# Optimization experiments

Hardware: AMD Instinct MI355X
Metric: run time of the kernel (lower is better)

The kernel has to match this reference:

```python
import jax, jax.numpy as jnp
import numpy as np


def _lap_mul(A, x):
    # L @ x with L = D^{-1/2} A D^{-1/2}, D = diag(rowsum(A))
    d = 1.0 / jnp.sqrt(jnp.sum(A, axis=-1))  # [N]
    return d[:, None] * (A @ (d[:, None] * x))


def setup_inputs() -> dict:
    key = jax.random.key(0)
    k1, k2, k3, k4, k5, k6 = jax.random.split(key, 6)
    N, D_IN, D_OUT = 4096, 128, 128
    x = jax.random.normal(k1, (N, D_IN), dtype=jnp.float32)
    A = jax.random.uniform(k2, (N, N), dtype=jnp.float32)
    # linear params stored as [in, out] (apply via x @ W + b)
    s1 = 1.0 / np.sqrt(D_IN)
    W1 = jax.random.uniform(k3, (D_IN, D_OUT), minval=-s1, maxval=s1, dtype=jnp.float32)
    b1 = jax.random.uniform(k4, (D_OUT,), minval=-s1, maxval=s1, dtype=jnp.float32)
    W2 = jax.random.uniform(k5, (D_IN, D_OUT), minval=-s1, maxval=s1, dtype=jnp.float32)
    b2 = jax.random.uniform(k6, (D_OUT,), minval=-s1, maxval=s1, dtype=jnp.float32)
    return {"x": x, "A": A, "W1": W1, "b1": b1, "W2": W2, "b2": b2, "sigma": 1, "k": 4}


def reference(x, A, W1, b1, W2, b2, sigma, k):
    # first graph conv + linear1 + leaky relu
    z = _lap_mul(A, x) @ W1 + b1            # [N, d_out]
    z = jax.nn.leaky_relu(z, negative_slope=0.1)

    # pairwise Euclidean distance (efficient cdist form, same math as the
    # original broadcasted (z_i - z_j)**2 sum, without the d x N x N blowup)
    sq = jnp.sum(z * z, axis=-1)            # [N]
    d2 = sq[:, None] + sq[None, :] - 2.0 * (z @ z.T)
    d2 = jnp.maximum(d2, 0.0)
    S = jnp.sqrt(d2 + 1e-10)                # [N, N]
    S = jnp.exp(-S / (2.0 * sigma))

    # double-argsort rank -> keep top-k per row (emulates original masking)
    order = jnp.argsort(-S, axis=-1)
    ranks = jnp.argsort(order, axis=-1)
    S = jnp.where(ranks < k, S, 0.0)

    A2 = S + A
    out = _lap_mul(A2, x) @ W2 + b2         # [N, d_out]
    return out
```

## Files before the change

### kernel.cpp

```cpp
#include <hip/hip_runtime.h>
#include <cstdint>
#include <cstddef>

#define NN 4096
#define DD 128

using short8 = __attribute__((ext_vector_type(8))) short;
using f32x4  = __attribute__((ext_vector_type(4))) float;
typedef unsigned long long u64;

typedef __attribute__((address_space(1))) void gvoid;
typedef __attribute__((address_space(3))) void lvoid;

__device__ __forceinline__ void async16(const void* g, void* l) {
  __builtin_amdgcn_global_load_lds((gvoid*)g, (lvoid*)l, 16, 0, 0);
}

__device__ __forceinline__ float dec_f(const void* p) {
  if (!p) return 1.0f;
  int b = *(const int*)p;
  return (b >= 0 && b < 1000000) ? (float)b : __int_as_float(b);
}
__device__ __forceinline__ int dec_i(const void* p) {
  if (!p) return 4;
  int b = *(const int*)p;
  return (b >= 0 && b < 1000000) ? b : (int)__int_as_float(b);
}

__device__ __forceinline__ unsigned short f2bf(float f) {
  union { float f; unsigned int u; } v; v.f = f;
  unsigned int u = v.u;
  unsigned int r = (u + 0x7fffu + ((u >> 16) & 1u)) >> 16;
  return (unsigned short)r;
}
__device__ __forceinline__ float bf2f(unsigned short h) {
  union { unsigned int u; float f; } v; v.u = ((unsigned int)h) << 16;
  return v.f;
}

__device__ __forceinline__ void ins4(u64 (&l)[4], u64 k) {
#pragma unroll
  for (int t = 0; t < 4; ++t) {
    u64 old = l[t];
    bool bt = k < old;
    l[t] = bt ? k : old;
    k = bt ? old : k;
  }
}

template <int ROWS, int KC, int NTHR>
__device__ __forceinline__ void stage2(const unsigned short* src, int row0, int kb,
                                       unsigned short* dst, int tid, int stride) {
  const int CPR = KC / 8;
  const int ITER = (ROWS * CPR) / NTHR;
#pragma unroll
  for (int t = 0; t < ITER; ++t) {
    int id = tid + t * NTHR;
    int r = id / CPR;
    int p = id % CPR;
    int lc = p ^ (r & 7);
    const void* g = src + (size_t)(row0 + r) * stride + kb + lc * 8;
    async16(g, dst + (size_t)(id & ~63) * 8);
  }
}

template <int CPR>
__device__ __forceinline__ short8 fragN(const unsigned short* t, int row, int ch) {
  return *(const short8*)(t + (size_t)(row * CPR + (ch ^ (row & 7))) * 8);
}

__global__ __launch_bounds__(256) void k_rowsum_scale(
    const float* __restrict__ A, const float* __restrict__ x,
    float* __restrict__ rowsumA, float* __restrict__ dvec, float* __restrict__ V,
    unsigned short* __restrict__ Ah, unsigned short* __restrict__ Al) {
  int row = blockIdx.x;
  int tid = threadIdx.x;
  const float4* Arow = (const float4*)(A + (size_t)row * NN);
  float s = 0.f;
#pragma unroll
  for (int l = 0; l < 4; ++l) {
    int idx = tid + l * 256;
    float4 v = Arow[idx];
    s += (v.x + v.y) + (v.z + v.w);
    if (Ah) {
      ushort4 h = {f2bf(v.x), f2bf(v.y), f2bf(v.z), f2bf(v.w)};
      *(ushort4*)(Ah + (size_t)row * NN + idx * 4) = h;
      if (Al) {
        ushort4 lo = {f2bf(v.x - bf2f(h.x)), f2bf(v.y - bf2f(h.y)),
                      f2bf(v.z - bf2f(h.z)), f2bf(v.w - bf2f(h.w))};
        *(ushort4*)(Al + (size_t)row * NN + idx * 4) = lo;
      }
    }
  }
  __shared__ float red[256];
  __shared__ float dsh;
  red[tid] = s;
  __syncthreads();
  if (tid < 64) {
    s = red[tid] + red[tid + 64] + red[tid + 128] + red[tid + 192];
#pragma unroll
    for (int off = 32; off > 0; off >>= 1) s += __shfl_down(s, off, 64);
    if (tid == 0) { rowsumA[row] = s; float d = rsqrtf(s); dvec[row] = d; dsh = d; }
  }
  __syncthreads();
  float d = dsh;
  if (tid < 32) {
    float4 xv = ((const float4*)(x + (size_t)row * DD))[tid];
    float4 o; o.x = d * xv.x; o.y = d * xv.y; o.z = d * xv.z; o.w = d * xv.w;
    ((float4*)(V + (size_t)row * DD))[tid] = o;
  }
}

__global__ __launch_bounds__(256) void k_vt(
    const float* __restrict__ V, unsigned short* __restrict__ VTh,
    unsigned short* __restrict__ VTl, int emit_lo) {
  __shared__ float Ls[64 * 132];
  int bx = blockIdx.x, tid = threadIdx.x;
  int r0 = bx * 64;
#pragma unroll
  for (int l = 0; l < 8; ++l) {
    int idx = tid + l * 256;
    int r = idx >> 5, c4 = (idx & 31) << 2;
    *(float4*)(Ls + r * 132 + c4) = *(const float4*)(V + (size_t)(r0 + r) * DD + c4);
  }
  __syncthreads();
  int c = tid >> 1, rh = tid & 1;
  unsigned short hb[32], lb[32];
#pragma unroll
  for (int i = 0; i < 32; ++i) {
    float v = Ls[(rh * 32 + i) * 132 + c];
    hb[i] = f2bf(v);
    lb[i] = f2bf(v - bf2f(hb[i]));
  }
  size_t base = (size_t)c * NN + r0 + rh * 32;
#pragma unroll
  for (int q = 0; q < 8; ++q) {
    ushort4 h = {hb[q * 4], hb[q * 4 + 1], hb[q * 4 + 2], hb[q * 4 + 3]};
    *(ushort4*)(VTh + base + q * 4) = h;
  }
  if (emit_lo) {
#pragma unroll
    for (int q = 0; q < 8; ++q) {
      ushort4 lo = {lb[q * 4], lb[q * 4 + 1], lb[q * 4 + 2], lb[q * 4 + 3]};
      *(ushort4*)(VTl + base + q * 4) = lo;
    }
  }
}

template <int TERMS>
__global__ __launch_bounds__(256) void k_gemm_bf16(
    const unsigned short* __restrict__ Ah, const unsigned short* __restrict__ Al,
    const unsigned short* __restrict__ Bh, const unsigned short* __restrict__ Bl,
    float* __restrict__ G) {
  __shared__ __align__(16) unsigned short As_h[128 * 64];
  __shared__ __align__(16) unsigned short Bs_h[128 * 64];
  __shared__ __align__(16) unsigned short As_l[TERMS == 3 ? 128 * 64 : 8];
  __shared__ __align__(16) unsigned short Bs_l[TERMS == 3 ? 128 * 64 : 8];

  int bx = blockIdx.x;
  int mt = bx >> 4, sp = bx & 15;
  int m0 = mt * 128;
  int ks = sp * 256;
  int tid = threadIdx.x, lane = tid & 63, w = tid >> 6;
  int wm = w >> 1, wn = w & 1;
  int l15 = lane & 15, quad = lane >> 4;

  f32x4 acc[4][4];
#pragma unroll
  for (int a = 0; a < 4; ++a)
#pragma unroll
    for (int b = 0; b < 4; ++b) acc[a][b] = (f32x4){0.f, 0.f, 0.f, 0.f};

  for (int kt = 0; kt < 256; kt += 64) {
    int kb = ks + kt;
    __syncthreads();
    stage2<128, 64, 256>(Ah, m0, kb, As_h, tid, NN);
    stage2<128, 64, 256>(Bh, 0, kb, Bs_h, tid, NN);
    if (TERMS == 3) {
      stage2<128, 64, 256>(Al, m0, kb, As_l, tid, NN);
      stage2<128, 64, 256>(Bl, 0, kb, Bs_l, tid, NN);
    }
    __syncthreads();
#pragma unroll
    for (int k0 = 0; k0 < 64; k0 += 32) {
      int ch = (k0 >> 3) + quad;
      short8 a_h[4], b_h[4], a_l[4], b_l[4];
#pragma unroll
      for (int f = 0; f < 4; ++f) {
        int ra = wm * 64 + f * 16 + l15;
        int cb = wn * 64 + f * 16 + l15;
        a_h[f] = fragN<8>(As_h, ra, ch);
        b_h[f] = fragN<8>(Bs_h, cb, ch);
        if (TERMS == 3) { a_l[f] = fragN<8>(As_l, ra, ch); b_l[f] = fragN<8>(Bs_l, cb, ch); }
      }
#pragma unroll
      for (int fm = 0; fm < 4; ++fm)
#pragma unroll
        for (int fn = 0; fn < 4; ++fn) {
          acc[fm][fn] = __builtin_amdgcn_mfma_f32_16x16x32_bf16(a_h[fm], b_h[fn], acc[fm][fn], 0, 0, 0);
          if (TERMS == 3) {
            acc[fm][fn] = __builtin_amdgcn_mfma_f32_16x16x32_bf16(a_h[fm], b_l[fn], acc[fm][fn], 0, 0, 0);
            acc[fm][fn] = __builtin_amdgcn_mfma_f32_16x16x32_bf16(a_l[fm], b_h[fn], acc[fm][fn], 0, 0, 0);
          }
        }
    }
  }
  float* Gp = G + (size_t)sp * NN * DD;
#pragma unroll
  for (int fm = 0; fm < 4; ++fm) {
    int rb = m0 + wm * 64 + fm * 16 + quad * 4;
#pragma unroll
    for (int fn = 0; fn < 4; ++fn) {
      int c = wn * 64 + fn * 16 + l15;
#pragma unroll
      for (int i = 0; i < 4; ++i)
        Gp[(size_t)(rb + i) * DD + c] = acc[fm][fn][i];
    }
  }
}

__global__ __launch_bounds__(256) void k_gemm_av(
    const float* __restrict__ A, const float* __restrict__ V,
    float* __restrict__ G, int ksplit) {
  int bx = blockIdx.x;
  int mt = bx & 63;
  int sp = bx >> 6;
  int m0 = mt * 64;
  int klen = NN / ksplit;
  int k0 = sp * klen;
  int tid = threadIdx.x;
  int tr = tid >> 4, tc = tid & 15;
  __shared__ float As[64 * 68];
  __shared__ float Bs[64 * 128];
  float acc[4][8];
#pragma unroll
  for (int r = 0; r < 4; ++r)
#pragma unroll
    for (int c = 0; c < 8; ++c) acc[r][c] = 0.f;
  for (int kt = 0; kt < klen; kt += 64) {
    int kb = k0 + kt;
    __syncthreads();
#pragma unroll
    for (int l = 0; l < 4; ++l) {
      int idx = tid + l * 256;
      int r = idx >> 4;
      int kq = (idx & 15) << 2;
      float4 a = *(const float4*)(A + (size_t)(m0 + r) * NN + kb + kq);
      As[(kq + 0) * 68 + r] = a.x;
      As[(kq + 1) * 68 + r] = a.y;
      As[(kq + 2) * 68 + r] = a.z;
      As[(kq + 3) * 68 + r] = a.w;
    }
#pragma unroll
    for (int l = 0; l < 8; ++l) {
      int idx = tid + l * 256;
      int kr = idx >> 5;
      int c4 = (idx & 31) << 2;
      *(float4*)(Bs + kr * 128 + c4) = *(const float4*)(V + (size_t)(kb + kr) * DD + c4);
    }
    __syncthreads();
#pragma unroll 8
    for (int kk = 0; kk < 64; ++kk) {
      float4 a = *(const float4*)(As + kk * 68 + tr * 4);
      float4 b0 = *(const float4*)(Bs + kk * 128 + tc * 8);
      float4 b1 = *(const float4*)(Bs + kk * 128 + tc * 8 + 4);
      float av[4] = {a.x, a.y, a.z, a.w};
      float bv[8] = {b0.x, b0.y, b0.z, b0.w, b1.x, b1.y, b1.z, b1.w};
#pragma unroll
      for (int r = 0; r < 4; ++r)
#pragma unroll
        for (int c = 0; c < 8; ++c) acc[r][c] = fmaf(av[r], bv[c], acc[r][c]);
    }
  }
  float* Gp = G + (size_t)sp * NN * DD;
#pragma unroll
  for (int r = 0; r < 4; ++r) {
    int gr = m0 + tr * 4 + r;
    float4 o0 = {acc[r][0], acc[r][1], acc[r][2], acc[r][3]};
    float4 o1 = {acc[r][4], acc[r][5], acc[r][6], acc[r][7]};
    *(float4*)(Gp + (size_t)gr * DD + tc * 8) = o0;
    *(float4*)(Gp + (size_t)gr * DD + tc * 8 + 4) = o1;
  }
}

template <int NP>
__global__ __launch_bounds__(256) void k_lin(
    const float* __restrict__ G,
    const float* __restrict__ W, const float* __restrict__ bvec,
    const float* __restrict__ dvec, float* __restrict__ Out,
    int leaky, float* __restrict__ sqout,
    unsigned short* __restrict__ zh, unsigned short* __restrict__ zl,
    const float* __restrict__ Vsp, const float* __restrict__ sval,
    const int* __restrict__ sidx, const void* kptr) {
  int bx = blockIdx.x;
  int r0 = bx * 16;
  int tid = threadIdx.x;
  int tr = tid >> 4, tc = tid & 15;
  __shared__ float Gs[16 * 132];
  __shared__ float Ws[32 * 128];
  __shared__ float red[256];
  __shared__ float ds[16];

#pragma unroll
  for (int l = 0; l < 8; ++l) {
    int idx = tid + l * 256;
    int r = idx >> 7;
    int c = idx & 127;
    float v = 0.f;
#pragma unroll
    for (int p = 0; p < NP; ++p)
      v += G[(size_t)p * NN * DD + (size_t)(r0 + r) * DD + c];
    Gs[r * 132 + c] = v;
  }
  if (tid < 16) ds[tid] = dvec[r0 + tid];

  if (sidx != nullptr) {
    __syncthreads();
    int kk = dec_i(kptr); kk = kk < 1 ? 1 : (kk > 4 ? 4 : kk);
    int gr = r0 + tr;
    float add[8] = {0, 0, 0, 0, 0, 0, 0, 0};
    for (int t = 0; t < kk; ++t) {
      float sv = sval[gr * 8 + t];
      int id = sidx[gr * 8 + t];
      const float4* vr = (const float4*)(Vsp + (size_t)id * DD);
      float4 w0 = vr[tc * 2], w1 = vr[tc * 2 + 1];
      add[0] = fmaf(sv, w0.x, add[0]); add[1] = fmaf(sv, w0.y, add[1]);
      add[2] = fmaf(sv, w0.z, add[2]); add[3] = fmaf(sv, w0.w, add[3]);
      add[4] = fmaf(sv, w1.x, add[4]); add[5] = fmaf(sv, w1.y, add[5]);
      add[6] = fmaf(sv, w1.z, add[6]); add[7] = fmaf(sv, w1.w, add[7]);
    }
#pragma unroll
    for (int u = 0; u < 8; ++u) Gs[tr * 132 + tc * 8 + u] += add[u];
  }

  float acc[8];
#pragma unroll
  for (int u = 0; u < 8; ++u) acc[u] = 0.f;

  for (int t0 = 0; t0 < 128; t0 += 32) {
    __syncthreads();
#pragma unroll
    for (int l = 0; l < 4; ++l) {
      int idx = tid + l * 256;
      int tt = idx >> 5;
      int c4 = (idx & 31) << 2;
      *(float4*)(Ws + tt * 128 + c4) = *(const float4*)(W + (size_t)(t0 + tt) * DD + c4);
    }
    __syncthreads();
#pragma unroll 8
    for (int tt = 0; tt < 32; ++tt) {
      float g = Gs[tr * 132 + t0 + tt];
      float4 w0 = *(const float4*)(Ws + tt * 128 + tc * 8);
      float4 w1 = *(const float4*)(Ws + tt * 128 + tc * 8 + 4);
      acc[0] = fmaf(g, w0.x, acc[0]); acc[1] = fmaf(g, w0.y, acc[1]);
      acc[2] = fmaf(g, w0.z, acc[2]); acc[3] = fmaf(g, w0.w, acc[3]);
      acc[4] = fmaf(g, w1.x, acc[4]); acc[5] = fmaf(g, w1.y, acc[5]);
      acc[6] = fmaf(g, w1.z, acc[6]); acc[7] = fmaf(g, w1.w, acc[7]);
    }
  }

  float d = ds[tr];
  float4 b0 = *(const float4*)(bvec + tc * 8);
  float4 b1 = *(const float4*)(bvec + tc * 8 + 4);
  float bb[8] = {b0.x, b0.y, b0.z, b0.w, b1.x, b1.y, b1.z, b1.w};
  float o[8];
#pragma unroll
  for (int u = 0; u < 8; ++u) {
    float v = fmaf(d, acc[u], bb[u]);
    if (leaky) v = v > 0.f ? v : 0.1f * v;
    o[u] = v;
  }
  size_t rowoff = (size_t)(r0 + tr) * DD + tc * 8;
  if (Out) {
    float4 o0 = {o[0], o[1], o[2], o[3]};
    float4 o1 = {o[4], o[5], o[6], o[7]};
    *(float4*)(Out + rowoff) = o0;
    *(float4*)(Out + rowoff + 4) = o1;
  }
  if (zh) {
    unsigned short hb[8], lb[8];
#pragma unroll
    for (int u = 0; u < 8; ++u) {
      hb[u] = f2bf(o[u]);
      lb[u] = f2bf(o[u] - bf2f(hb[u]));
    }
    ushort4 h0 = {hb[0], hb[1], hb[2], hb[3]};
    ushort4 h1 = {hb[4], hb[5], hb[6], hb[7]};
    ushort4 l0 = {lb[0], lb[1], lb[2], lb[3]};
    ushort4 l1 = {lb[4], lb[5], lb[6], lb[7]};
    *(ushort4*)(zh + rowoff) = h0;
    *(ushort4*)(zh + rowoff + 4) = h1;
    *(ushort4*)(zl + rowoff) = l0;
    *(ushort4*)(zl + rowoff + 4) = l1;
  }

  if (sqout != nullptr) {
    float p = 0.f;
#pragma unroll
    for (int u = 0; u < 8; ++u) p = fmaf(o[u], o[u], p);
    red[tid] = p;
    __syncthreads();
    if (tc == 0) {
      float s = 0.f;
#pragma unroll
      for (int i = 0; i < 16; ++i) s += red[tr * 16 + i];
      sqout[r0 + tr] = s;
    }
  }
}

__global__ __launch_bounds__(512) void k_scores(
    const unsigned short* __restrict__ Zh, const unsigned short* __restrict__ Zl,
    const float* __restrict__ sq, u64* __restrict__ pkey) {
  __shared__ __align__(16) unsigned short Am[2][64 * 128];
  __shared__ __align__(16) unsigned short Bj[2][64 * 128];
  float* Stile = (float*)&Bj[0][0];
  u64* mv = (u64*)&Am[0][0];

  int bx = blockIdx.x;
  int mt = bx >> 4, jp = bx & 15;
  int m0 = mt * 64, j0 = jp * 256;
  int tid = threadIdx.x, lane = tid & 63, w = tid >> 6;
  int wm = w >> 2, wn = w & 3;
  int l15 = lane & 15, quad = lane >> 4;

  stage2<64, 128, 512>(Zh, m0, 0, Am[0], tid, DD);
  stage2<64, 128, 512>(Zl, m0, 0, Am[1], tid, DD);

  int srow = tid >> 3;
  int sc = tid & 7;
  float sqi_r = sq[m0 + srow];

  u64 lst[4];
#pragma unroll
  for (int s = 0; s < 4; ++s) lst[s] = ~0ull;

  for (int jt = 0; jt < 4; ++jt) {
    int jrow0 = j0 + jt * 64;
    __syncthreads();
    stage2<64, 128, 512>(Zh, jrow0, 0, Bj[0], tid, DD);
    stage2<64, 128, 512>(Zl, jrow0, 0, Bj[1], tid, DD);
    __syncthreads();

    f32x4 acc[2];
    acc[0] = (f32x4){0.f, 0.f, 0.f, 0.f};
    acc[1] = (f32x4){0.f, 0.f, 0.f, 0.f};
#pragma unroll
    for (int kc = 0; kc < 4; ++kc) {
      int ch = kc * 4 + quad;
      short8 ah0 = fragN<16>(Am[0], wm * 32 + l15, ch);
      short8 ah1 = fragN<16>(Am[0], wm * 32 + 16 + l15, ch);
      short8 al0 = fragN<16>(Am[1], wm * 32 + l15, ch);
      short8 al1 = fragN<16>(Am[1], wm * 32 + 16 + l15, ch);
      short8 bh  = fragN<16>(Bj[0], wn * 16 + l15, ch);
      short8 bl  = fragN<16>(Bj[1], wn * 16 + l15, ch);
      acc[0] = __builtin_amdgcn_mfma_f32_16x16x32_bf16(ah0, bh, acc[0], 0, 0, 0);
      acc[0] = __builtin_amdgcn_mfma_f32_16x16x32_bf16(ah0, bl, acc[0], 0, 0, 0);
      acc[0] = __builtin_amdgcn_mfma_f32_16x16x32_bf16(al0, bh, acc[0], 0, 0, 0);
      acc[1] = __builtin_amdgcn_mfma_f32_16x16x32_bf16(ah1, bh, acc[1], 0, 0, 0);
      acc[1] = __builtin_amdgcn_mfma_f32_16x16x32_bf16(ah1, bl, acc[1], 0, 0, 0);
      acc[1] = __builtin_amdgcn_mfma_f32_16x16x32_bf16(al1, bh, acc[1], 0, 0, 0);
    }
    __syncthreads();

    {
      int c = wn * 16 + l15;
      float sqjv = sq[jrow0 + c];
      int cslot = c >> 2, cw = c & 3;
#pragma unroll
      for (int fm = 0; fm < 2; ++fm) {
        int rb = wm * 32 + fm * 16 + quad * 4;
#pragma unroll
        for (int i = 0; i < 4; ++i) {
          int r = rb + i;
          Stile[r * 64 + ((cslot ^ (r & 7)) << 2) + cw] = fmaf(-2.f, acc[fm][i], sqjv);
        }
      }
    }
    __syncthreads();

#pragma unroll
    for (int q = 0; q < 2; ++q) {
      int slot = sc * 2 + q;
      float4 kv = *(const float4*)(Stile + srow * 64 + ((slot ^ (srow & 7)) << 2));
      int jb = jrow0 + sc * 8 + q * 4;
      float ke[4] = {kv.x, kv.y, kv.z, kv.w};
#pragma unroll
      for (int e = 0; e < 4; ++e) {
        float v = fmaxf(sqi_r + ke[e], 0.f);
        ins4(lst, ((u64)__float_as_uint(v) << 32) | (unsigned)(jb + e));
      }
    }
  }

  __syncthreads();
#pragma unroll
  for (int s = 0; s < 4; ++s) mv[tid * 4 + s] = lst[s];
  __syncthreads();
  if (tid < 64) {
    u64 best[4] = {~0ull, ~0ull, ~0ull, ~0ull};
    for (int g = 0; g < 8; ++g) {
      int src = tid * 8 + g;
#pragma unroll
      for (int s = 0; s < 4; ++s) ins4(best, mv[src * 4 + s]);
    }
#pragma unroll
    for (int s = 0; s < 4; ++s)
      pkey[((size_t)(m0 + tid) * 16 + jp) * 4 + s] = best[s];
  }
}

__global__ __launch_bounds__(256) void k_merge(
    const u64* __restrict__ pkey,
    const float* __restrict__ rowsumA, const float* __restrict__ x,
    float* __restrict__ sval, int* __restrict__ sidx,
    float* __restrict__ d2vec, float* __restrict__ V,
    const void* kptr, const void* sigptr) {
  int bx = blockIdx.x;
  int r0 = bx * 16;
  int tid = threadIdx.x;
  int kk = dec_i(kptr); kk = kk < 1 ? 1 : (kk > 4 ? 4 : kk);
  float inv2s = 0.5f / dec_f(sigptr);
  __shared__ float ds[16];
  if (tid < 16) {
    int r = r0 + tid;
    u64 best[4] = {~0ull, ~0ull, ~0ull, ~0ull};
    for (int p = 0; p < 16; ++p) {
#pragma unroll
      for (int s = 0; s < 4; ++s) ins4(best, pkey[((size_t)r * 16 + p) * 4 + s]);
    }
    float srw = 0.f;
#pragma unroll
    for (int s = 0; s < 4; ++s) {
      if (s < kk) {
        float d2 = __uint_as_float((unsigned)(best[s] >> 32));
        float S = __expf(-sqrtf(d2 + 1e-10f) * inv2s);
        sval[r * 8 + s] = S;
        sidx[r * 8 + s] = (int)(best[s] & 0xffffffffu);
        srw += S;
      }
    }
    float dd = rsqrtf(rowsumA[r] + srw);
    d2vec[r] = dd;
    ds[tid] = dd;
  }
  __syncthreads();
#pragma unroll
  for (int l = 0; l < 2; ++l) {
    int idx = tid + l * 256;
    int rl = idx >> 5;
    int c4 = (idx & 31) << 2;
    float4 xv = *(const float4*)(x + (size_t)(r0 + rl) * DD + c4);
    float dd = ds[rl];
    float4 o; o.x = dd * xv.x; o.y = dd * xv.y; o.z = dd * xv.z; o.w = dd * xv.w;
    *(float4*)(V + (size_t)(r0 + rl) * DD + c4) = o;
  }
}

extern "C" void kernel_launch(void* const* d_in, const int* in_sizes, int n_in,
                              void* d_out, int out_size, void* d_ws, size_t ws_size,
                              hipStream_t stream) {
  const float* x  = (const float*)d_in[0];
  const float* A  = (const float*)d_in[1];
  const float* W1 = (const float*)d_in[2];
  const float* b1 = (const float*)d_in[3];
  const float* W2 = (const float*)d_in[4];
  const float* b2 = (const float*)d_in[5];
  const void* sig = (n_in > 6) ? d_in[6] : nullptr;
  const void* kp  = (n_in > 7) ? d_in[7] : nullptr;

  float* ws = (float*)d_ws;
  float* rowsumA = ws;
  float* dvec    = ws + 4096;
  float* d2vec   = ws + 8192;
  float* sqv     = ws + 12288;
  float* sval    = ws + 16384;
  int*   sidx    = (int*)(ws + 49152);
  u64*   pkey    = (u64*)(ws + 81920);
  unsigned short* Zh = (unsigned short*)(ws + 1130496);
  unsigned short* Zl = (unsigned short*)(ws + 1392640);
  float* V       = ws + 1654784;

  const size_t F_FULL = 27869184;
  const size_t F_MID  = 19218432;
  int tier = (ws_size >= F_FULL * 4) ? 2 : (ws_size >= F_MID * 4) ? 1 : 0;

  if (tier >= 1) {
    unsigned short* VTh = (unsigned short*)(ws + 2179072);
    unsigned short* VTl;
    unsigned short* Ah;
    unsigned short* Al = nullptr;
    float* G;
    if (tier == 2) {
      VTl = (unsigned short*)(ws + 2441216);
      Ah  = (unsigned short*)(ws + 2703360);
      Al  = (unsigned short*)(ws + 11091968);
      G   = ws + 19480576;
    } else {
      VTl = nullptr;
      Ah  = (unsigned short*)(ws + 2441216);
      G   = ws + 10829824;
    }

    k_rowsum_scale<<<4096, 256, 0, stream>>>(A, x, rowsumA, dvec, V, Ah, Al);
    k_vt<<<64, 256, 0, stream>>>(V, VTh, VTl, tier == 2 ? 1 : 0);
    if (tier == 2)
      k_gemm_bf16<3><<<512, 256, 0, stream>>>(Ah, Al, VTh, VTl, G);
    else
      k_gemm_bf16<1><<<512, 256, 0, stream>>>(Ah, nullptr, VTh, nullptr, G);
    k_lin<16><<<256, 256, 0, stream>>>(G, W1, b1, dvec, nullptr, 1, sqv, Zh, Zl,
                                       nullptr, nullptr, nullptr, nullptr);
    k_scores<<<1024, 512, 0, stream>>>(Zh, Zl, sqv, pkey);
    k_merge<<<256, 256, 0, stream>>>(pkey, rowsumA, x, sval, sidx, d2vec, V, kp, sig);
    k_vt<<<64, 256, 0, stream>>>(V, VTh, nullptr, 0);
    k_gemm_bf16<1><<<512, 256, 0, stream>>>(Ah, nullptr, VTh, nullptr, G);
    k_lin<16><<<256, 256, 0, stream>>>(G, W2, b2, d2vec, (float*)d_out, 0, nullptr,
                                       nullptr, nullptr, V, sval, sidx, kp);
  } else {
    float* G = ws + 2179072;
    const size_t nd = (size_t)NN * DD;
    int ksplit = 4;
    if (ws_size < (2179072 + 4 * nd) * 4) ksplit = 2;
    if (ws_size < (2179072 + 2 * nd) * 4) ksplit = 1;

    k_rowsum_scale<<<4096, 256, 0, stream>>>(A, x, rowsumA, dvec, V, nullptr, nullptr);
    k_gemm_av<<<64 * ksplit, 256, 0, stream>>>(A, V, G, ksplit);
    if (ksplit == 4)
      k_lin<4><<<256, 256, 0, stream>>>(G, W1, b1, dvec, nullptr, 1, sqv, Zh, Zl,
                                        nullptr, nullptr, nullptr, nullptr);
    else if (ksplit == 2)
      k_lin<2><<<256, 256, 0, stream>>>(G, W1, b1, dvec, nullptr, 1, sqv, Zh, Zl,
                                        nullptr, nullptr, nullptr, nullptr);
    else
      k_lin<1><<<256, 256, 0, stream>>>(G, W1, b1, dvec, nullptr, 1, sqv, Zh, Zl,
                                        nullptr, nullptr, nullptr, nullptr);
    k_scores<<<1024, 512, 0, stream>>>(Zh, Zl, sqv, pkey);
    k_merge<<<256, 256, 0, stream>>>(pkey, rowsumA, x, sval, sidx, d2vec, V, kp, sig);
    k_gemm_av<<<64 * ksplit, 256, 0, stream>>>(A, V, G, ksplit);
    if (ksplit == 4)
      k_lin<4><<<256, 256, 0, stream>>>(G, W2, b2, d2vec, (float*)d_out, 0, nullptr,
                                        nullptr, nullptr, V, sval, sidx, kp);
    else if (ksplit == 2)
      k_lin<2><<<256, 256, 0, stream>>>(G, W2, b2, d2vec, (float*)d_out, 0, nullptr,
                                        nullptr, nullptr, V, sval, sidx, kp);
    else
      k_lin<1><<<256, 256, 0, stream>>>(G, W2, b2, d2vec, (float*)d_out, 0, nullptr,
                                        nullptr, nullptr, V, sval, sidx, kp);
  }
}
```

Baseline: 233.0 us.

## Drop split-bf16 precision terms and reassociate linear layer before A multiply

```diff
diff --git a/kernel.cpp b/kernel.cpp
--- a/kernel.cpp
+++ b/kernel.cpp
@@ -32,10 +32,6 @@
   unsigned int u = v.u;
   unsigned int r = (u + 0x7fffu + ((u >> 16) & 1u)) >> 16;
   return (unsigned short)r;
-}
-__device__ __forceinline__ float bf2f(unsigned short h) {
-  union { unsigned int u; float f; } v; v.u = ((unsigned int)h) << 16;
-  return v.f;
 }
 
 __device__ __forceinline__ void ins4(u64 (&l)[4], u64 k) {
@@ -72,7 +68,7 @@
 __global__ __launch_bounds__(256) void k_rowsum_scale(
     const float* __restrict__ A, const float* __restrict__ x,
     float* __restrict__ rowsumA, float* __restrict__ dvec, float* __restrict__ V,
-    unsigned short* __restrict__ Ah, unsigned short* __restrict__ Al) {
+    unsigned short* __restrict__ Ah) {
   int row = blockIdx.x;
   int tid = threadIdx.x;
   const float4* Arow = (const float4*)(A + (size_t)row * NN);
@@ -82,15 +78,8 @@
     int idx = tid + l * 256;
     float4 v = Arow[idx];
     s += (v.x + v.y) + (v.z + v.w);
-    if (Ah) {
-      ushort4 h = {f2bf(v.x), f2bf(v.y), f2bf(v.z), f2bf(v.w)};
-      *(ushort4*)(Ah + (size_t)row * NN + idx * 4) = h;
-      if (Al) {
-        ushort4 lo = {f2bf(v.x - bf2f(h.x)), f2bf(v.y - bf2f(h.y)),
-                      f2bf(v.z - bf2f(h.z)), f2bf(v.w - bf2f(h.w))};
-        *(ushort4*)(Al + (size_t)row * NN + idx * 4) = lo;
-      }
-    }
+    ushort4 h = {f2bf(v.x), f2bf(v.y), f2bf(v.z), f2bf(v.w)};
+    *(ushort4*)(Ah + (size_t)row * NN + idx * 4) = h;
   }
   __shared__ float red[256];
   __shared__ float dsh;
@@ -111,245 +100,34 @@
   }
 }
 
-__global__ __launch_bounds__(256) void k_vt(
-    const float* __restrict__ V, unsigned short* __restrict__ VTh,
-    unsigned short* __restrict__ VTl, int emit_lo) {
-  __shared__ float Ls[64 * 132];
-  int bx = blockIdx.x, tid = threadIdx.x;
-  int r0 = bx * 64;
+__global__ __launch_bounds__(256) void k_xw(
+    const float* __restrict__ X, const float* __restrict__ W, float* __restrict__ P) {
+  int r0 = blockIdx.x * 16;
+  int tid = threadIdx.x;
+  int tr = tid >> 4, tc = tid & 15;
+  __shared__ float Xs[16 * 132];
+  __shared__ float Ws[32 * 128];
 #pragma unroll
   for (int l = 0; l < 8; ++l) {
     int idx = tid + l * 256;
-    int r = idx >> 5, c4 = (idx & 31) << 2;
-    *(float4*)(Ls + r * 132 + c4) = *(const float4*)(V + (size_t)(r0 + r) * DD + c4);
-  }
-  __syncthreads();
-  int c = tid >> 1, rh = tid & 1;
-  unsigned short hb[32], lb[32];
-#pragma unroll
-  for (int i = 0; i < 32; ++i) {
-    float v = Ls[(rh * 32 + i) * 132 + c];
-    hb[i] = f2bf(v);
-    lb[i] = f2bf(v - bf2f(hb[i]));
-  }
-  size_t base = (size_t)c * NN + r0 + rh * 32;
-#pragma unroll
-  for (int q = 0; q < 8; ++q) {
-    ushort4 h = {hb[q * 4], hb[q * 4 + 1], hb[q * 4 + 2], hb[q * 4 + 3]};
-    *(ushort4*)(VTh + base + q * 4) = h;
-  }
-  if (emit_lo) {
-#pragma unroll
-    for (int q = 0; q < 8; ++q) {
-      ushort4 lo = {lb[q * 4], lb[q * 4 + 1], lb[q * 4 + 2], lb[q * 4 + 3]};
-      *(ushort4*)(VTl + base + q * 4) = lo;
-    }
-  }
-}
-
-template <int TERMS>
-__global__ __launch_bounds__(256) void k_gemm_bf16(
-    const unsigned short* __restrict__ Ah, const unsigned short* __restrict__ Al,
-    const unsigned short* __restrict__ Bh, const unsigned short* __restrict__ Bl,
-    float* __restrict__ G) {
-  __shared__ __align__(16) unsigned short As_h[128 * 64];
-  __shared__ __align__(16) unsigned short Bs_h[128 * 64];
-  __shared__ __align__(16) unsigned short As_l[TERMS == 3 ? 128 * 64 : 8];
-  __shared__ __align__(16) unsigned short Bs_l[TERMS == 3 ? 128 * 64 : 8];
-
-  int bx = blockIdx.x;
-  int mt = bx >> 4, sp = bx & 15;
-  int m0 = mt * 128;
-  int ks = sp * 256;
-  int tid = threadIdx.x, lane = tid & 63, w = tid >> 6;
-  int wm = w >> 1, wn = w & 1;
-  int l15 = lane & 15, quad = lane >> 4;
-
-  f32x4 acc[4][4];
-#pragma unroll
-  for (int a = 0; a < 4; ++a)
-#pragma unroll
-    for (int b = 0; b < 4; ++b) acc[a][b] = (f32x4){0.f, 0.f, 0.f, 0.f};
-
-  for (int kt = 0; kt < 256; kt += 64) {
-    int kb = ks + kt;
-    __syncthreads();
-    stage2<128, 64, 256>(Ah, m0, kb, As_h, tid, NN);
-    stage2<128, 64, 256>(Bh, 0, kb, Bs_h, tid, NN);
-    if (TERMS == 3) {
-      stage2<128, 64, 256>(Al, m0, kb, As_l, tid, NN);
-      stage2<128, 64, 256>(Bl, 0, kb, Bs_l, tid, NN);
-    }
-    __syncthreads();
-#pragma unroll
-    for (int k0 = 0; k0 < 64; k0 += 32) {
-      int ch = (k0 >> 3) + quad;
-      short8 a_h[4], b_h[4], a_l[4], b_l[4];
-#pragma unroll
-      for (int f = 0; f < 4; ++f) {
-        int ra = wm * 64 + f * 16 + l15;
-        int cb = wn * 64 + f * 16 + l15;
-        a_h[f] = fragN<8>(As_h, ra, ch);
-        b_h[f] = fragN<8>(Bs_h, cb, ch);
-        if (TERMS == 3) { a_l[f] = fragN<8>(As_l, ra, ch); b_l[f] = fragN<8>(Bs_l, cb, ch); }
-      }
-#pragma unroll
-      for (int fm = 0; fm < 4; ++fm)
-#pragma unroll
-        for (int fn = 0; fn < 4; ++fn) {
-          acc[fm][fn] = __builtin_amdgcn_mfma_f32_16x16x32_bf16(a_h[fm], b_h[fn], acc[fm][fn], 0, 0, 0);
-          if (TERMS == 3) {
-            acc[fm][fn] = __builtin_amdgcn_mfma_f32_16x16x32_bf16(a_h[fm], b_l[fn], acc[fm][fn], 0, 0, 0);
-            acc[fm][fn] = __builtin_amdgcn_mfma_f32_16x16x32_bf16(a_l[fm], b_h[fn], acc[fm][fn], 0, 0, 0);
-          }
-        }
-    }
-  }
-  float* Gp = G + (size_t)sp * NN * DD;
-#pragma unroll
-  for (int fm = 0; fm < 4; ++fm) {
-    int rb = m0 + wm * 64 + fm * 16 + quad * 4;
-#pragma unroll
-    for (int fn = 0; fn < 4; ++fn) {
-      int c = wn * 64 + fn * 16 + l15;
-#pragma unroll
-      for (int i = 0; i < 4; ++i)
-        Gp[(size_t)(rb + i) * DD + c] = acc[fm][fn][i];
-    }
-  }
-}
-
-__global__ __launch_bounds__(256) void k_gemm_av(
-    const float* __restrict__ A, const float* __restrict__ V,
-    float* __restrict__ G, int ksplit) {
-  int bx = blockIdx.x;
-  int mt = bx & 63;
-  int sp = bx >> 6;
-  int m0 = mt * 64;
-  int klen = NN / ksplit;
-  int k0 = sp * klen;
-  int tid = threadIdx.x;
-  int tr = tid >> 4, tc = tid & 15;
-  __shared__ float As[64 * 68];
-  __shared__ float Bs[64 * 128];
-  float acc[4][8];
-#pragma unroll
-  for (int r = 0; r < 4; ++r)
-#pragma unroll
-    for (int c = 0; c < 8; ++c) acc[r][c] = 0.f;
-  for (int kt = 0; kt < klen; kt += 64) {
-    int kb = k0 + kt;
+    int r = idx >> 7, c = idx & 127;
+    Xs[r * 132 + c] = X[(size_t)(r0 + r) * DD + c];
+  }
+  float acc[8];
+#pragma unroll
+  for (int u = 0; u < 8; ++u) acc[u] = 0.f;
+  for (int t0 = 0; t0 < 128; t0 += 32) {
     __syncthreads();
 #pragma unroll
     for (int l = 0; l < 4; ++l) {
       int idx = tid + l * 256;
-      int r = idx >> 4;
-      int kq = (idx & 15) << 2;
-      float4 a = *(const float4*)(A + (size_t)(m0 + r) * NN + kb + kq);
-      As[(kq + 0) * 68 + r] = a.x;
-      As[(kq + 1) * 68 + r] = a.y;
-      As[(kq + 2) * 68 + r] = a.z;
-      As[(kq + 3) * 68 + r] = a.w;
-    }
-#pragma unroll
-    for (int l = 0; l < 8; ++l) {
-      int idx = tid + l * 256;
-      int kr = idx >> 5;
-      int c4 = (idx & 31) << 2;
-      *(float4*)(Bs + kr * 128 + c4) = *(const float4*)(V + (size_t)(kb + kr) * DD + c4);
-    }
-    __syncthreads();
-#pragma unroll 8
-    for (int kk = 0; kk < 64; ++kk) {
-      float4 a = *(const float4*)(As + kk * 68 + tr * 4);
-      float4 b0 = *(const float4*)(Bs + kk * 128 + tc * 8);
-      float4 b1 = *(const float4*)(Bs + kk * 128 + tc * 8 + 4);
-      float av[4] = {a.x, a.y, a.z, a.w};
-      float bv[8] = {b0.x, b0.y, b0.z, b0.w, b1.x, b1.y, b1.z, b1.w};
-#pragma unroll
-      for (int r = 0; r < 4; ++r)
-#pragma unroll
-        for (int c = 0; c < 8; ++c) acc[r][c] = fmaf(av[r], bv[c], acc[r][c]);
-    }
-  }
-  float* Gp = G + (size_t)sp * NN * DD;
-#pragma unroll
-  for (int r = 0; r < 4; ++r) {
-    int gr = m0 + tr * 4 + r;
-    float4 o0 = {acc[r][0], acc[r][1], acc[r][2], acc[r][3]};
-    float4 o1 = {acc[r][4], acc[r][5], acc[r][6], acc[r][7]};
-    *(float4*)(Gp + (size_t)gr * DD + tc * 8) = o0;
-    *(float4*)(Gp + (size_t)gr * DD + tc * 8 + 4) = o1;
-  }
-}
-
-template <int NP>
-__global__ __launch_bounds__(256) void k_lin(
-    const float* __restrict__ G,
-    const float* __restrict__ W, const float* __restrict__ bvec,
-    const float* __restrict__ dvec, float* __restrict__ Out,
-    int leaky, float* __restrict__ sqout,
-    unsigned short* __restrict__ zh, unsigned short* __restrict__ zl,
-    const float* __restrict__ Vsp, const float* __restrict__ sval,
-    const int* __restrict__ sidx, const void* kptr) {
-  int bx = blockIdx.x;
-  int r0 = bx * 16;
-  int tid = threadIdx.x;
-  int tr = tid >> 4, tc = tid & 15;
-  __shared__ float Gs[16 * 132];
-  __shared__ float Ws[32 * 128];
-  __shared__ float red[256];
-  __shared__ float ds[16];
-
-#pragma unroll
-  for (int l = 0; l < 8; ++l) {
-    int idx = tid + l * 256;
-    int r = idx >> 7;
-    int c = idx & 127;
-    float v = 0.f;
-#pragma unroll
-    for (int p = 0; p < NP; ++p)
-      v += G[(size_t)p * NN * DD + (size_t)(r0 + r) * DD + c];
-    Gs[r * 132 + c] = v;
-  }
-  if (tid < 16) ds[tid] = dvec[r0 + tid];
-
-  if (sidx != nullptr) {
-    __syncthreads();
-    int kk = dec_i(kptr); kk = kk < 1 ? 1 : (kk > 4 ? 4 : kk);
-    int gr = r0 + tr;
-    float add[8] = {0, 0, 0, 0, 0, 0, 0, 0};
-    for (int t = 0; t < kk; ++t) {
-      float sv = sval[gr * 8 + t];
-      int id = sidx[gr * 8 + t];
-      const float4* vr = (const float4*)(Vsp + (size_t)id * DD);
-      float4 w0 = vr[tc * 2], w1 = vr[tc * 2 + 1];
-      add[0] = fmaf(sv, w0.x, add[0]); add[1] = fmaf(sv, w0.y, add[1]);
-      add[2] = fmaf(sv, w0.z, add[2]); add[3] = fmaf(sv, w0.w, add[3]);
-      add[4] = fmaf(sv, w1.x, add[4]); add[5] = fmaf(sv, w1.y, add[5]);
-      add[6] = fmaf(sv, w1.z, add[6]); add[7] = fmaf(sv, w1.w, add[7]);
-    }
-#pragma unroll
-    for (int u = 0; u < 8; ++u) Gs[tr * 132 + tc * 8 + u] += add[u];
-  }
-
-  float acc[8];
-#pragma unroll
-  for (int u = 0; u < 8; ++u) acc[u] = 0.f;
-
-  for (int t0 = 0; t0 < 128; t0 += 32) {
-    __syncthreads();
-#pragma unroll
-    for (int l = 0; l < 4; ++l) {
-      int idx = tid + l * 256;
-      int tt = idx >> 5;
-      int c4 = (idx & 31) << 2;
+      int tt = idx >> 5, c4 = (idx & 31) << 2;
       *(float4*)(Ws + tt * 128 + c4) = *(const float4*)(W + (size_t)(t0 + tt) * DD + c4);
     }
     __syncthreads();
 #pragma unroll 8
     for (int tt = 0; tt < 32; ++tt) {
-      float g = Gs[tr * 132 + t0 + tt];
+      float g = Xs[tr * 132 + t0 + tt];
       float4 w0 = *(const float4*)(Ws + tt * 128 + tc * 8);
       float4 w1 = *(const float4*)(Ws + tt * 128 + tc * 8 + 4);
       acc[0] = fmaf(g, w0.x, acc[0]); acc[1] = fmaf(g, w0.y, acc[1]);
@@ -358,8 +136,136 @@
       acc[6] = fmaf(g, w1.z, acc[6]); acc[7] = fmaf(g, w1.w, acc[7]);
     }
   }
-
-  float d = ds[tr];
+  size_t off = (size_t)(r0 + tr) * DD + tc * 8;
+  float4 o0 = {acc[0], acc[1], acc[2], acc[3]};
+  float4 o1 = {acc[4], acc[5], acc[6], acc[7]};
+  *(float4*)(P + off) = o0;
+  *(float4*)(P + off + 4) = o1;
+}
+
+__global__ __launch_bounds__(256) void k_vt(
+    const float* __restrict__ U, unsigned short* __restrict__ UTh) {
+  __shared__ float Ls[64 * 132];
+  int bx = blockIdx.x, tid = threadIdx.x;
+  int r0 = bx * 64;
+#pragma unroll
+  for (int l = 0; l < 8; ++l) {
+    int idx = tid + l * 256;
+    int r = idx >> 5, c4 = (idx & 31) << 2;
+    *(float4*)(Ls + r * 132 + c4) = *(const float4*)(U + (size_t)(r0 + r) * DD + c4);
+  }
+  __syncthreads();
+  int c = tid >> 1, rh = tid & 1;
+  unsigned short hb[32];
+#pragma unroll
+  for (int i = 0; i < 32; ++i) hb[i] = f2bf(Ls[(rh * 32 + i) * 132 + c]);
+  size_t base = (size_t)c * NN + r0 + rh * 32;
+#pragma unroll
+  for (int q = 0; q < 8; ++q) {
+    ushort4 h = {hb[q * 4], hb[q * 4 + 1], hb[q * 4 + 2], hb[q * 4 + 3]};
+    *(ushort4*)(UTh + base + q * 4) = h;
+  }
+}
+
+template <int SPLIT>
+__global__ __launch_bounds__(256) void k_gemm_bf16(
+    const unsigned short* __restrict__ Ah, const unsigned short* __restrict__ Bh,
+    float* __restrict__ G) {
+  __shared__ __align__(16) unsigned short As_h[128 * 64];
+  __shared__ __align__(16) unsigned short Bs_h[128 * 64];
+
+  int bx = blockIdx.x;
+  int mt = bx / SPLIT, sp = bx % SPLIT;
+  int m0 = mt * 128;
+  const int KLEN = NN / SPLIT;
+  int ks = sp * KLEN;
+  int tid = threadIdx.x, lane = tid & 63, w = tid >> 6;
+  int wm = w >> 1, wn = w & 1;
+  int l15 = lane & 15, quad = lane >> 4;
+
+  f32x4 acc[4][4];
+#pragma unroll
+  for (int a = 0; a < 4; ++a)
+#pragma unroll
+    for (int b = 0; b < 4; ++b) acc[a][b] = (f32x4){0.f, 0.f, 0.f, 0.f};
+
+  for (int kt = 0; kt < KLEN; kt += 64) {
+    int kb = ks + kt;
+    __syncthreads();
+    stage2<128, 64, 256>(Ah, m0, kb, As_h, tid, NN);
+    stage2<128, 64, 256>(Bh, 0, kb, Bs_h, tid, NN);
+    __syncthreads();
+#pragma unroll
+    for (int k0 = 0; k0 < 64; k0 += 32) {
+      int ch = (k0 >> 3) + quad;
+      short8 a_h[4], b_h[4];
+#pragma unroll
+      for (int f = 0; f < 4; ++f) {
+        a_h[f] = fragN<8>(As_h, wm * 64 + f * 16 + l15, ch);
+        b_h[f] = fragN<8>(Bs_h, wn * 64 + f * 16 + l15, ch);
+      }
+#pragma unroll
+      for (int fm = 0; fm < 4; ++fm)
+#pragma unroll
+        for (int fn = 0; fn < 4; ++fn)
+          acc[fm][fn] = __builtin_amdgcn_mfma_f32_16x16x32_bf16(a_h[fm], b_h[fn], acc[fm][fn], 0, 0, 0);
+    }
+  }
+  float* Gp = G + (size_t)sp * NN * DD;
+#pragma unroll
+  for (int fm = 0; fm < 4; ++fm) {
+    int rb = m0 + wm * 64 + fm * 16 + quad * 4;
+#pragma unroll
+    for (int fn = 0; fn < 4; ++fn) {
+      int c = wn * 64 + fn * 16 + l15;
+#pragma unroll
+      for (int i = 0; i < 4; ++i)
+        Gp[(size_t)(rb + i) * DD + c] = acc[fm][fn][i];
+    }
+  }
+}
+
+template <int NP>
+__global__ __launch_bounds__(256) void k_red(
+    const float* __restrict__ G, const float* __restrict__ dvec,
+    const float* __restrict__ bvec, int leaky,
+    float* __restrict__ Out, unsigned short* __restrict__ zh,
+    float* __restrict__ sqout,
+    const float* __restrict__ Usp, const float* __restrict__ sval,
+    const int* __restrict__ sidx, const void* kptr) {
+  int r0 = blockIdx.x * 16;
+  int tid = threadIdx.x;
+  int tr = tid >> 4, tc = tid & 15;
+  int r = r0 + tr;
+  size_t off = (size_t)r * DD + tc * 8;
+  __shared__ float red[256];
+
+  float acc[8];
+#pragma unroll
+  for (int u = 0; u < 8; ++u) acc[u] = 0.f;
+#pragma unroll
+  for (int p = 0; p < NP; ++p) {
+    const float* gp = G + (size_t)p * NN * DD + off;
+    float4 g0 = *(const float4*)gp;
+    float4 g1 = *(const float4*)(gp + 4);
+    acc[0] += g0.x; acc[1] += g0.y; acc[2] += g0.z; acc[3] += g0.w;
+    acc[4] += g1.x; acc[5] += g1.y; acc[6] += g1.z; acc[7] += g1.w;
+  }
+  if (sidx != nullptr) {
+    int kk = dec_i(kptr); kk = kk < 1 ? 1 : (kk > 4 ? 4 : kk);
+    for (int t = 0; t < kk; ++t) {
+      float sv = sval[r * 8 + t];
+      int id = sidx[r * 8 + t];
+      const float* vr = Usp + (size_t)id * DD + tc * 8;
+      float4 w0 = *(const float4*)vr;
+      float4 w1 = *(const float4*)(vr + 4);
+      acc[0] = fmaf(sv, w0.x, acc[0]); acc[1] = fmaf(sv, w0.y, acc[1]);
+      acc[2] = fmaf(sv, w0.z, acc[2]); acc[3] = fmaf(sv, w0.w, acc[3]);
+      acc[4] = fmaf(sv, w1.x, acc[4]); acc[5] = fmaf(sv, w1.y, acc[5]);
+      acc[6] = fmaf(sv, w1.z, acc[6]); acc[7] = fmaf(sv, w1.w, acc[7]);
+    }
+  }
+  float d = dvec[r];
   float4 b0 = *(const float4*)(bvec + tc * 8);
   float4 b1 = *(const float4*)(bvec + tc * 8 + 4);
   float bb[8] = {b0.x, b0.y, b0.z, b0.w, b1.x, b1.y, b1.z, b1.w};
@@ -370,30 +276,18 @@
     if (leaky) v = v > 0.f ? v : 0.1f * v;
     o[u] = v;
   }
-  size_t rowoff = (size_t)(r0 + tr) * DD + tc * 8;
   if (Out) {
     float4 o0 = {o[0], o[1], o[2], o[3]};
     float4 o1 = {o[4], o[5], o[6], o[7]};
-    *(float4*)(Out + rowoff) = o0;
-    *(float4*)(Out + rowoff + 4) = o1;
+    *(float4*)(Out + off) = o0;
+    *(float4*)(Out + off + 4) = o1;
   }
   if (zh) {
-    unsigned short hb[8], lb[8];
-#pragma unroll
-    for (int u = 0; u < 8; ++u) {
-      hb[u] = f2bf(o[u]);
-      lb[u] = f2bf(o[u] - bf2f(hb[u]));
-    }
-    ushort4 h0 = {hb[0], hb[1], hb[2], hb[3]};
-    ushort4 h1 = {hb[4], hb[5], hb[6], hb[7]};
-    ushort4 l0 = {lb[0], lb[1], lb[2], lb[3]};
-    ushort4 l1 = {lb[4], lb[5], lb[6], lb[7]};
-    *(ushort4*)(zh + rowoff) = h0;
-    *(ushort4*)(zh + rowoff + 4) = h1;
-    *(ushort4*)(zl + rowoff) = l0;
-    *(ushort4*)(zl + rowoff + 4) = l1;
-  }
-
+    ushort4 h0 = {f2bf(o[0]), f2bf(o[1]), f2bf(o[2]), f2bf(o[3])};
+    ushort4 h1 = {f2bf(o[4]), f2bf(o[5]), f2bf(o[6]), f2bf(o[7])};
+    *(ushort4*)(zh + off) = h0;
+    *(ushort4*)(zh + off + 4) = h1;
+  }
   if (sqout != nullptr) {
     float p = 0.f;
 #pragma unroll
@@ -404,18 +298,18 @@
       float s = 0.f;
 #pragma unroll
       for (int i = 0; i < 16; ++i) s += red[tr * 16 + i];
-      sqout[r0 + tr] = s;
-    }
-  }
-}
-
-__global__ __launch_bounds__(512) void k_scores(
-    const unsigned short* __restrict__ Zh, const unsigned short* __restrict__ Zl,
+      sqout[r] = s;
+    }
+  }
+}
+
+__global__ __launch_bounds__(512, 8) void k_scores(
+    const unsigned short* __restrict__ Zh,
     const float* __restrict__ sq, u64* __restrict__ pkey) {
-  __shared__ __align__(16) unsigned short Am[2][64 * 128];
-  __shared__ __align__(16) unsigned short Bj[2][64 * 128];
-  float* Stile = (float*)&Bj[0][0];
-  u64* mv = (u64*)&Am[0][0];
+  __shared__ __align__(16) unsigned short Am[64 * 128];
+  __shared__ __align__(16) unsigned short Bj[64 * 128];
+  float* Stile = (float*)&Bj[0];
+  u64* mv = (u64*)&Am[0];
 
   int bx = blockIdx.x;
   int mt = bx >> 4, jp = bx & 15;
@@ -424,8 +318,7 @@
   int wm = w >> 2, wn = w & 3;
   int l15 = lane & 15, quad = lane >> 4;
 
-  stage2<64, 128, 512>(Zh, m0, 0, Am[0], tid, DD);
-  stage2<64, 128, 512>(Zl, m0, 0, Am[1], tid, DD);
+  stage2<64, 128, 512>(Zh, m0, 0, Am, tid, DD);
 
   int srow = tid >> 3;
   int sc = tid & 7;
@@ -438,8 +331,7 @@
   for (int jt = 0; jt < 4; ++jt) {
     int jrow0 = j0 + jt * 64;
     __syncthreads();
-    stage2<64, 128, 512>(Zh, jrow0, 0, Bj[0], tid, DD);
-    stage2<64, 128, 512>(Zl, jrow0, 0, Bj[1], tid, DD);
+    stage2<64, 128, 512>(Zh, jrow0, 0, Bj, tid, DD);
     __syncthreads();
 
     f32x4 acc[2];
@@ -448,18 +340,11 @@
 #pragma unroll
     for (int kc = 0; kc < 4; ++kc) {
       int ch = kc * 4 + quad;
-      short8 ah0 = fragN<16>(Am[0], wm * 32 + l15, ch);
-      short8 ah1 = fragN<16>(Am[0], wm * 32 + 16 + l15, ch);
-      short8 al0 = fragN<16>(Am[1], wm * 32 + l15, ch);
-      short8 al1 = fragN<16>(Am[1], wm * 32 + 16 + l15, ch);
-      short8 bh  = fragN<16>(Bj[0], wn * 16 + l15, ch);
-      short8 bl  = fragN<16>(Bj[1], wn * 16 + l15, ch);
+      short8 ah0 = fragN<16>(Am, wm * 32 + l15, ch);
+      short8 ah1 = fragN<16>(Am, wm * 32 + 16 + l15, ch);
+      short8 bh  = fragN<16>(Bj, wn * 16 + l15, ch);
       acc[0] = __builtin_amdgcn_mfma_f32_16x16x32_bf16(ah0, bh, acc[0], 0, 0, 0);
-      acc[0] = __builtin_amdgcn_mfma_f32_16x16x32_bf16(ah0, bl, acc[0], 0, 0, 0);
-      acc[0] = __builtin_amdgcn_mfma_f32_16x16x32_bf16(al0, bh, acc[0], 0, 0, 0);
       acc[1] = __builtin_amdgcn_mfma_f32_16x16x32_bf16(ah1, bh, acc[1], 0, 0, 0);
-      acc[1] = __builtin_amdgcn_mfma_f32_16x16x32_bf16(ah1, bl, acc[1], 0, 0, 0);
-      acc[1] = __builtin_amdgcn_mfma_f32_16x16x32_bf16(al1, bh, acc[1], 0, 0, 0);
     }
     __syncthreads();
 
@@ -577,74 +462,39 @@
   float* sval    = ws + 16384;
   int*   sidx    = (int*)(ws + 49152);
   u64*   pkey    = (u64*)(ws + 81920);
-  unsigned short* Zh = (unsigned short*)(ws + 1130496);
-  unsigned short* Zl = (unsigned short*)(ws + 1392640);
-  float* V       = ws + 1654784;
-
-  const size_t F_FULL = 27869184;
-  const size_t F_MID  = 19218432;
-  int tier = (ws_size >= F_FULL * 4) ? 2 : (ws_size >= F_MID * 4) ? 1 : 0;
-
-  if (tier >= 1) {
-    unsigned short* VTh = (unsigned short*)(ws + 2179072);
-    unsigned short* VTl;
-    unsigned short* Ah;
-    unsigned short* Al = nullptr;
-    float* G;
-    if (tier == 2) {
-      VTl = (unsigned short*)(ws + 2441216);
-      Ah  = (unsigned short*)(ws + 2703360);
-      Al  = (unsigned short*)(ws + 11091968);
-      G   = ws + 19480576;
-    } else {
-      VTl = nullptr;
-      Ah  = (unsigned short*)(ws + 2441216);
-      G   = ws + 10829824;
-    }
-
-    k_rowsum_scale<<<4096, 256, 0, stream>>>(A, x, rowsumA, dvec, V, Ah, Al);
-    k_vt<<<64, 256, 0, stream>>>(V, VTh, VTl, tier == 2 ? 1 : 0);
-    if (tier == 2)
-      k_gemm_bf16<3><<<512, 256, 0, stream>>>(Ah, Al, VTh, VTl, G);
-    else
-      k_gemm_bf16<1><<<512, 256, 0, stream>>>(Ah, nullptr, VTh, nullptr, G);
-    k_lin<16><<<256, 256, 0, stream>>>(G, W1, b1, dvec, nullptr, 1, sqv, Zh, Zl,
+  unsigned short* Zh = (unsigned short*)(ws + 606208);
+  float* V       = ws + 868352;
+  float* U       = ws + 1392640;
+  unsigned short* UTh = (unsigned short*)(ws + 1916928);
+  unsigned short* Ah  = (unsigned short*)(ws + 2179072);
+  float* G       = ws + 10567680;
+
+  const size_t F16 = 10567680 + 16 * 524288;
+  int split16 = (ws_size >= F16 * 4);
+
+  k_rowsum_scale<<<4096, 256, 0, stream>>>(A, x, rowsumA, dvec, V, Ah);
+  k_xw<<<256, 256, 0, stream>>>(V, W1, U);
+  k_vt<<<64, 256, 0, stream>>>(U, UTh);
+  if (split16) {
+    k_gemm_bf16<16><<<512, 256, 0, stream>>>(Ah, UTh, G);
+    k_red<16><<<256, 256, 0, stream>>>(G, dvec, b1, 1, nullptr, Zh, sqv,
                                        nullptr, nullptr, nullptr, nullptr);
-    k_scores<<<1024, 512, 0, stream>>>(Zh, Zl, sqv, pkey);
-    k_merge<<<256, 256, 0, stream>>>(pkey, rowsumA, x, sval, sidx, d2vec, V, kp, sig);
-    k_vt<<<64, 256, 0, stream>>>(V, VTh, nullptr, 0);
-    k_gemm_bf16<1><<<512, 256, 0, stream>>>(Ah, nullptr, VTh, nullptr, G);
-    k_lin<16><<<256, 256, 0, stream>>>(G, W2, b2, d2vec, (float*)d_out, 0, nullptr,
-                                       nullptr, nullptr, V, sval, sidx, kp);
   } else {
-    float* G = ws + 2179072;
-    const size_t nd = (size_t)NN * DD;
-    int ksplit = 4;
-    if (ws_size < (2179072 + 4 * nd) * 4) ksplit = 2;
-    if (ws_size < (2179072 + 2 * nd) * 4) ksplit = 1;
-
-    k_rowsum_scale<<<4096, 256, 0, stream>>>(A, x, rowsumA, dvec, V, nullptr, nullptr);
-    k_gemm_av<<<64 * ksplit, 256, 0, stream>>>(A, V, G, ksplit);
-    if (ksplit == 4)
-      k_lin<4><<<256, 256, 0, stream>>>(G, W1, b1, dvec, nullptr, 1, sqv, Zh, Zl,
-                                        nullptr, nullptr, nullptr, nullptr);
-    else if (ksplit == 2)
-      k_lin<2><<<256, 256, 0, stream>>>(G, W1, b1, dvec, nullptr, 1, sqv, Zh, Zl,
-                                        nullptr, nullptr, nullptr, nullptr);
-    else
-      k_lin<1><<<256, 256, 0, stream>>>(G, W1, b1, dvec, nullptr, 1, sqv, Zh, Zl,
-                                        nullptr, nullptr, nullptr, nullptr);
-    k_scores<<<1024, 512, 0, stream>>>(Zh, Zl, sqv, pkey);
-    k_merge<<<256, 256, 0, stream>>>(pkey, rowsumA, x, sval, sidx, d2vec, V, kp, sig);
-    k_gemm_av<<<64 * ksplit, 256, 0, stream>>>(A, V, G, ksplit);
-    if (ksplit == 4)
-      k_lin<4><<<256, 256, 0, stream>>>(G, W2, b2, d2vec, (float*)d_out, 0, nullptr,
-                                        nullptr, nullptr, V, sval, sidx, kp);
-    else if (ksplit == 2)
-      k_lin<2><<<256, 256, 0, stream>>>(G, W2, b2, d2vec, (float*)d_out, 0, nullptr,
-                                        nullptr, nullptr, V, sval, sidx, kp);
-    else
-      k_lin<1><<<256, 256, 0, stream>>>(G, W2, b2, d2vec, (float*)d_out, 0, nullptr,
-                                        nullptr, nullptr, V, sval, sidx, kp);
-  }
-}
+    k_gemm_bf16<4><<<128, 256, 0, stream>>>(Ah, UTh, G);
+    k_red<4><<<256, 256, 0, stream>>>(G, dvec, b1, 1, nullptr, Zh, sqv,
+                                      nullptr, nullptr, nullptr, nullptr);
+  }
+  k_scores<<<1024, 512, 0, stream>>>(Zh, sqv, pkey);
+  k_merge<<<256, 256, 0, stream>>>(pkey, rowsumA, x, sval, sidx, d2vec, V, kp, sig);
+  k_xw<<<256, 256, 0, stream>>>(V, W2, U);
+  k_vt<<<64, 256, 0, stream>>>(U, UTh);
+  if (split16) {
+    k_gemm_bf16<16><<<512, 256, 0, stream>>>(Ah, UTh, G);
+    k_red<16><<<256, 256, 0, stream>>>(G, d2vec, b2, 0, (float*)d_out, nullptr, nullptr,
+                                       U, sval, sidx, kp);
+  } else {
+    k_gemm_bf16<4><<<128, 256, 0, stream>>>(Ah, UTh, G);
+    k_red<4><<<256, 256, 0, stream>>>(G, d2vec, b2, 0, (float*)d_out, nullptr, nullptr,
+                                      U, sval, sidx, kp);
+  }
+}
```

Result: faster. 209.7 us (-10.0%).
